# Optimization experiments

Measured on AMD Instinct MI355X. Metric: run time of the kernel, lower is better.

The kernel has to match this reference:

```python
import jax, jax.numpy as jnp
import numpy as np

D_MODEL = 1024
N_HEADS = 16
D_H = D_MODEL // N_HEADS
B, T = 4, 2048
NEG_INF = jnp.finfo(jnp.float32).min


def setup_inputs() -> dict:
    key = jax.random.key(0)
    ks = jax.random.split(key, 9)
    s = 1.0 / np.sqrt(D_MODEL)
    inp = {
        "x": jax.random.normal(ks[0], (B, T, D_MODEL), dtype=jnp.float32),
        "pad_mask": jnp.zeros((B, T), dtype=bool),
        "Wq": jax.random.uniform(ks[1], (D_MODEL, D_MODEL), jnp.float32, -s, s),
        "bq": jax.random.uniform(ks[2], (D_MODEL,), jnp.float32, -s, s),
        "Wk": jax.random.uniform(ks[3], (D_MODEL, D_MODEL), jnp.float32, -s, s),
        "bk": jax.random.uniform(ks[4], (D_MODEL,), jnp.float32, -s, s),
        "Wv": jax.random.uniform(ks[5], (D_MODEL, D_MODEL), jnp.float32, -s, s),
        "bv": jax.random.uniform(ks[6], (D_MODEL,), jnp.float32, -s, s),
        "Wo": jax.random.uniform(ks[7], (D_MODEL, D_MODEL), jnp.float32, -s, s),
        "bo": jax.random.uniform(ks[8], (D_MODEL,), jnp.float32, -s, s),
    }
    return inp


def reference(x, pad_mask, Wq, bq, Wk, bk, Wv, bv, Wo, bo):
    b, t, _ = x.shape
    # torch Linear: y = x @ W.T + b
    def proj(W, bias):
        y = jnp.einsum("btd,ed->bte", x, W) + bias
        return y.reshape(b, t, N_HEADS, D_H).transpose(0, 2, 1, 3)  # (B,H,T,d_h)

    Q, K, V = proj(Wq, bq), proj(Wk, bk), proj(Wv, bv)
    S = jnp.einsum("bhqd,bhkd->bhqk", Q, K) / jnp.sqrt(jnp.float32(D_H))
    causal = jnp.triu(jnp.ones((t, t), dtype=bool), k=1)[None, None]
    S = jnp.where(causal, NEG_INF, S)
    S = jnp.where(pad_mask[:, None, None, :], NEG_INF, S)
    A = jax.nn.softmax(S, axis=-1)
    Y = jnp.einsum("bhqk,bhkd->bhqd", A, V)
    Y = Y.transpose(0, 2, 1, 3).reshape(b, t, D_MODEL)
    O = jnp.einsum("btd,ed->bte", Y, Wo) + bo
    return O
```

## Files before the change

kernel.cpp:

```cpp
#include <hip/hip_runtime.h>
#include <stdint.h>
#include <stddef.h>

#define Tq 2048
#define DM 1024

typedef unsigned short u16;
typedef __bf16 bf16x8 __attribute__((ext_vector_type(8)));
typedef float f32x4 __attribute__((ext_vector_type(4)));
typedef unsigned short u16x8 __attribute__((ext_vector_type(8)));
typedef unsigned short u16x4 __attribute__((ext_vector_type(4)));

__device__ __forceinline__ float bf2f(u16 h) {
    union { unsigned int u; float f; } c; c.u = ((unsigned int)h) << 16; return c.f;
}
__device__ __forceinline__ u16 f2bf(float f) {
    union { float f; unsigned int u; } c; c.f = f;
    unsigned int u = c.u;
    return (u16)((u + 0x7fffu + ((u >> 16) & 1u)) >> 16);
}

#define GLD(gp, lp) __builtin_amdgcn_global_load_lds(                                  \
        (const __attribute__((address_space(1))) void*)(gp),                           \
        (__attribute__((address_space(3))) void*)(lp), 16, 0, 0)

__device__ __forceinline__ int sniff_fp32(const u16* xs) {
    const int lane = threadIdx.x & 63;
    const u16 u = xs[lane];
    const int e = (u >> 7) & 0xFF;
    unsigned long long m = __ballot(e >= 160);
    return __popcll(m) >= 4;
}

__device__ __forceinline__ void cvt_body(const void* src, u16* dst, int i0, int fmt) {
    if (fmt) {
        const float* s = (const float*)src;
        float4 a = *(const float4*)(s + i0);
        float4 b = *(const float4*)(s + i0 + 4);
        u16x8 o;
        o[0] = f2bf(a.x); o[1] = f2bf(a.y); o[2] = f2bf(a.z); o[3] = f2bf(a.w);
        o[4] = f2bf(b.x); o[5] = f2bf(b.y); o[6] = f2bf(b.z); o[7] = f2bf(b.w);
        *(u16x8*)(dst + i0) = o;
    } else {
        *(u16x8*)(dst + i0) = *(const u16x8*)((const u16*)src + i0);
    }
}

__global__ void cvt_all(const void* __restrict__ x,
                        const void* s0, const void* s1, const void* s2, const void* s3,
                        const void* t0, const void* t1, const void* t2, const void* t3,
                        u16* __restrict__ xc, u16* __restrict__ dstW, float* __restrict__ dstB,
                        const u16* __restrict__ xs, int* flag) {
    const int fmt = sniff_fp32(xs);
    int bx = blockIdx.x;
    if (bx < 4096) {
        if (bx == 0 && threadIdx.x == 0) *flag = fmt;
        const int i0 = (bx * 256 + threadIdx.x) * 8;
        cvt_body(x, xc, i0, fmt);
    } else {
        bx -= 4096;
        const int wsel = bx >> 9;
        const int bi   = bx & 511;
        const void* s = (wsel == 0) ? s0 : (wsel == 1) ? s1 : (wsel == 2) ? s2 : s3;
        u16* d = dstW + (size_t)wsel * (DM * DM);
        const int i0 = (bi * 256 + threadIdx.x) * 8;
        cvt_body(s, d, i0, fmt);
        if (bi == 0) {
            const void* bs = (wsel == 0) ? t0 : (wsel == 1) ? t1 : (wsel == 2) ? t2 : t3;
            float* db = dstB + (size_t)wsel * DM;
            const int j0 = threadIdx.x * 4;
            if (fmt) {
                *(float4*)(db + j0) = *(const float4*)((const float*)bs + j0);
            } else {
                const u16* ss = (const u16*)bs;
                db[j0+0] = bf2f(ss[j0+0]); db[j0+1] = bf2f(ss[j0+1]);
                db[j0+2] = bf2f(ss[j0+2]); db[j0+3] = bf2f(ss[j0+3]);
            }
        }
    }
}

__global__ __launch_bounds__(256, 2) void gemm_bt(
    const u16* __restrict__ A,
    const u16* __restrict__ W0, const u16* __restrict__ W1, const u16* __restrict__ W2,
    const float* __restrict__ b0, const float* __restrict__ b1, const float* __restrict__ b2,
    u16* o0, u16* o1, u16* o2,
    const int* __restrict__ flag, int mode)
{
    __shared__ u16 Alds[128 * 64];
    __shared__ u16 Blds[128 * 64];

    const int K = DM;
    const int i = blockIdx.x;
    const int j = blockIdx.y;
    const int which = (mode == 0) ? (j >> 3) : 0;
    const u16* W      = (which == 0) ? W0 : (which == 1) ? W1 : W2;
    const float* bias = (which == 0) ? b0 : (which == 1) ? b1 : b2;
    u16* out          = (which == 0) ? o0 : (which == 1) ? o1 : o2;
    const int jn = (mode == 0) ? (j & 7) : j;
    const int m0 = i * 128, n0 = jn * 128;
    const int ofmt = (mode == 1) ? *flag : 0;

    const int tid = threadIdx.x;
    const int w = tid >> 6, lane = tid & 63;
    const int l4 = lane & 15, quad = lane >> 4;
    const int wrow = w >> 1, wcol = w & 1;

    f32x4 acc[4][4] = {};

    for (int k0 = 0; k0 < K; k0 += 64) {
        __syncthreads();
#pragma unroll
        for (int c = 0; c < 4; ++c) {
            const int u   = w * 1024 + c * 4096;
            const int off = u + lane * 16;
            const int row = off >> 7;
            const int col = (off & 127) >> 1;
            GLD(A + (size_t)(m0 + row) * K + k0 + col, (char*)Alds + u);
            GLD(W + (size_t)(n0 + row) * K + k0 + col, (char*)Blds + u);
        }
        __syncthreads();
#pragma unroll
        for (int c = 0; c < 2; ++c) {
            bf16x8 af[4], bfr[4];
#pragma unroll
            for (int r = 0; r < 4; ++r)
                af[r] = *(const bf16x8*)&Alds[(wrow*64 + r*16 + l4) * 64 + c*32 + quad*8];
#pragma unroll
            for (int n = 0; n < 4; ++n)
                bfr[n] = *(const bf16x8*)&Blds[(wcol*64 + n*16 + l4) * 64 + c*32 + quad*8];
#pragma unroll
            for (int r = 0; r < 4; ++r)
#pragma unroll
                for (int n = 0; n < 4; ++n)
                    acc[r][n] = __builtin_amdgcn_mfma_f32_16x16x32_bf16(af[r], bfr[n], acc[r][n], 0, 0, 0);
        }
    }

#pragma unroll
    for (int n = 0; n < 4; ++n) {
        const int col = n0 + wcol*64 + n*16 + l4;
        const float bv = bias[col];
#pragma unroll
        for (int r = 0; r < 4; ++r) {
            const int mb = m0 + wrow*64 + r*16 + quad*4;
            if (mode == 0 && which == 2) {
                const int b = mb >> 11, t0 = mb & 2047;
                const int h = col >> 6, d = col & 63;
                u16x4 pk;
#pragma unroll
                for (int reg = 0; reg < 4; ++reg) pk[reg] = f2bf(acc[r][n][reg] + bv);
                *(u16x4*)&out[((size_t)(b*16 + h) * 64 + d) * 2048 + t0] = pk;
            } else {
#pragma unroll
                for (int reg = 0; reg < 4; ++reg) {
                    const int m = mb + reg;
                    const float val = acc[r][n][reg] + bv;
                    if (mode == 0) {
                        const int b = m >> 11, t = m & 2047;
                        const int h = col >> 6, d = col & 63;
                        out[(size_t)((b*16 + h) * 2048 + t) * 64 + d] = f2bf(val);
                    } else if (ofmt) {
                        ((float*)out)[(size_t)m * DM + col] = val;
                    } else {
                        out[(size_t)m * DM + col] = f2bf(val);
                    }
                }
            }
        }
    }
}

#define LSTR 72

__global__ __launch_bounds__(256, 2) void attn4(
    const u16* __restrict__ Qb, const u16* __restrict__ Kb, const u16* __restrict__ VT,
    const unsigned char* __restrict__ pad,
    u16* __restrict__ Y)
{
    __shared__ u16 Klds[2][64 * LSTR];
    __shared__ u16 Vtl [2][64 * LSTR];
    __shared__ u16 Pl  [4][64 * LSTR];
    __shared__ unsigned char padl[2][64];

    const int nb = blockIdx.y;
    const int bh = blockIdx.x;
    const int b = bh >> 4, h = bh & 15;
    const u16* Qp  = Qb + (size_t)bh * (Tq * 64);
    const u16* Kp  = Kb + (size_t)bh * (Tq * 64);
    const u16* VTp = VT + (size_t)bh * (64 * Tq);

    const int tid = threadIdx.x;
    const int w = tid >> 6, lane = tid & 63;
    const int l4 = lane & 15, quad = lane >> 4;

    const int qt[4] = { nb, nb + 8, 23 - nb, 31 - nb };

    bf16x8 qf[4][2];
#pragma unroll
    for (int g = 0; g < 4; ++g) {
        const u16* r = Qp + (size_t)(qt[g] * 64 + w * 16 + l4) * 64 + quad * 8;
        qf[g][0] = *(const bf16x8*)r;
        qf[g][1] = *(const bf16x8*)(r + 32);
    }

    f32x4 o[4][4] = {};
    float l[4][4] = {};

    const int srow = tid >> 2;
    const int sc   = (tid & 3) * 16;

    u16x8 kr0, kr1, vr0, vr1; unsigned char pr = 0;
    {
        const u16* kg = Kp + (size_t)srow * 64 + sc;
        kr0 = *(const u16x8*)kg; kr1 = *(const u16x8*)(kg + 8);
        const u16* vg = VTp + (size_t)srow * Tq + sc;
        vr0 = *(const u16x8*)vg; vr1 = *(const u16x8*)(vg + 8);
        if (tid < 64) pr = pad[(size_t)b * Tq + tid];
    }
    *(u16x8*)&Klds[0][srow * LSTR + sc]     = kr0;
    *(u16x8*)&Klds[0][srow * LSTR + sc + 8] = kr1;
    *(u16x8*)&Vtl [0][srow * LSTR + sc]     = vr0;
    *(u16x8*)&Vtl [0][srow * LSTR + sc + 8] = vr1;
    if (tid < 64) padl[0][tid] = pr;

    const float SC = 0.18033688011112042f;
    const int ktmax = qt[3];

    for (int kt = 0; kt <= ktmax; ++kt) {
        const int cur = kt & 1;
        const int k0 = kt * 64;
        __syncthreads();
        if (kt < ktmax) {
            const u16* kg = Kp + (size_t)(k0 + 64 + srow) * 64 + sc;
            kr0 = *(const u16x8*)kg; kr1 = *(const u16x8*)(kg + 8);
            const u16* vg = VTp + (size_t)srow * Tq + k0 + 64 + sc;
            vr0 = *(const u16x8*)vg; vr1 = *(const u16x8*)(vg + 8);
            if (tid < 64) pr = pad[(size_t)b * Tq + k0 + 64 + tid];
        }

        const bool anypad = __any((int)(padl[cur][lane] != 0));

        bf16x8 kf[2][4];
#pragma unroll
        for (int c = 0; c < 2; ++c)
#pragma unroll
            for (int n = 0; n < 4; ++n)
                kf[c][n] = *(const bf16x8*)&Klds[cur][(n * 16 + l4) * LSTR + c * 32 + quad * 8];

#pragma unroll
        for (int g = 0; g < 4; ++g) {
            if (kt > qt[g]) continue;
            f32x4 sacc[4] = {};
            __builtin_amdgcn_s_setprio(1);
#pragma unroll
            for (int c = 0; c < 2; ++c)
#pragma unroll
                for (int n = 0; n < 4; ++n)
                    sacc[n] = __builtin_amdgcn_mfma_f32_16x16x32_bf16(qf[g][c], kf[c][n], sacc[n], 0, 0, 0);
            __builtin_amdgcn_s_setprio(0);
            u16* Pg = &Pl[g][0];
            if (kt == qt[g] || anypad) {
                bool pm[4];
#pragma unroll
                for (int n = 0; n < 4; ++n) pm[n] = (padl[cur][n * 16 + l4] != 0);
                const int qr = qt[g] * 64 + w * 16 + quad * 4;
#pragma unroll
                for (int r = 0; r < 4; ++r) {
                    float rs = 0.f;
#pragma unroll
                    for (int n = 0; n < 4; ++n) {
                        const int kgi = k0 + n * 16 + l4;
                        const bool msk = (kgi > qr + r) || pm[n];
                        const float p = msk ? 0.0f : exp2f(sacc[n][r] * SC);
                        rs += p;
                        *(__bf16*)&Pg[(w * 16 + quad * 4 + r) * LSTR + n * 16 + l4] = (__bf16)p;
                    }
                    l[g][r] += rs;
                }
            } else {
#pragma unroll
                for (int r = 0; r < 4; ++r) {
                    float rs = 0.f;
#pragma unroll
                    for (int n = 0; n < 4; ++n) {
                        const float p = exp2f(sacc[n][r] * SC);
                        rs += p;
                        *(__bf16*)&Pg[(w * 16 + quad * 4 + r) * LSTR + n * 16 + l4] = (__bf16)p;
                    }
                    l[g][r] += rs;
                }
            }
        }

        bf16x8 vf[2][4];
#pragma unroll
        for (int c = 0; c < 2; ++c)
#pragma unroll
            for (int t = 0; t < 4; ++t)
                vf[c][t] = *(const bf16x8*)&Vtl[cur][(t * 16 + l4) * LSTR + c * 32 + quad * 8];

#pragma unroll
        for (int g = 0; g < 4; ++g) {
            if (kt > qt[g]) continue;
            __builtin_amdgcn_s_setprio(1);
#pragma unroll
            for (int c = 0; c < 2; ++c) {
                bf16x8 pf = *(const bf16x8*)&Pl[g][(w * 16 + l4) * LSTR + c * 32 + quad * 8];
#pragma unroll
                for (int t = 0; t < 4; ++t)
                    o[g][t] = __builtin_amdgcn_mfma_f32_16x16x32_bf16(pf, vf[c][t], o[g][t], 0, 0, 0);
            }
            __builtin_amdgcn_s_setprio(0);
        }

        if (kt < ktmax) {
            *(u16x8*)&Klds[cur ^ 1][srow * LSTR + sc]     = kr0;
            *(u16x8*)&Klds[cur ^ 1][srow * LSTR + sc + 8] = kr1;
            *(u16x8*)&Vtl [cur ^ 1][srow * LSTR + sc]     = vr0;
            *(u16x8*)&Vtl [cur ^ 1][srow * LSTR + sc + 8] = vr1;
            if (tid < 64) padl[cur ^ 1][tid] = pr;
        }
    }

#pragma unroll
    for (int g = 0; g < 4; ++g)
#pragma unroll
        for (int r = 0; r < 4; ++r)
#pragma unroll
            for (int s = 1; s < 16; s <<= 1)
                l[g][r] += __shfl_xor(l[g][r], s);

#pragma unroll
    for (int g = 0; g < 4; ++g)
#pragma unroll
        for (int r = 0; r < 4; ++r) {
            const float inv = 1.0f / l[g][r];
            u16* y = Y + (size_t)(b * Tq + (qt[g] * 64 + w * 16 + quad * 4 + r)) * DM + h * 64;
#pragma unroll
            for (int t = 0; t < 4; ++t)
                *(__bf16*)&y[t * 16 + l4] = (__bf16)(o[g][t][r] * inv);
        }
}

extern "C" void kernel_launch(void* const* d_in, const int* in_sizes, int n_in,
                              void* d_out, int out_size, void* d_ws, size_t ws_size,
                              hipStream_t stream) {
    const void* x  = d_in[0];
    const unsigned char* pad = (const unsigned char*)d_in[1];
    const void* Wq = d_in[2];
    const void* bq = d_in[3];
    const void* Wk = d_in[4];
    const void* bk = d_in[5];
    const void* Wv = d_in[6];
    const void* bv = d_in[7];
    const void* Wo = d_in[8];
    const void* bo = d_in[9];
    const u16* xs = (const u16*)x;

    const size_t NEL = (size_t)8192 * 1024;
    const size_t WEL = (size_t)1024 * 1024;

    int* flag   = (int*)d_ws;
    u16* base16 = (u16*)((char*)d_ws + 256);
    u16* xc     = base16;
    u16* Wc     = base16 + NEL;
    float* bf_  = (float*)(base16 + NEL + 4*WEL);
    u16* Qb     = (u16*)(bf_ + 4096);
    u16* Kb     = Qb + NEL;
    u16* VT     = Kb + NEL;
    u16* Yb     = xc;

    cvt_all<<<dim3(6144), 256, 0, stream>>>(x, Wq, Wk, Wv, Wo, bq, bk, bv, bo,
                                            xc, Wc, bf_, xs, flag);

    gemm_bt<<<dim3(64, 24), 256, 0, stream>>>(xc, Wc, Wc + WEL, Wc + 2*WEL,
                                              bf_, bf_ + 1024, bf_ + 2048,
                                              Qb, Kb, VT, flag, 0);
    attn4<<<dim3(64, 8), 256, 0, stream>>>(Qb, Kb, VT, pad, Yb);
    gemm_bt<<<dim3(64, 8), 256, 0, stream>>>(Yb, Wc + 3*WEL, Wc + 3*WEL, Wc + 3*WEL,
                                             bf_ + 3072, bf_ + 3072, bf_ + 3072,
                                             (u16*)d_out, nullptr, nullptr, flag, 1);
}
```

Baseline: 278.1 us.

## Rewrite projection GEMM with 128x256 tiles, double-buffered LDS, swizzle, and folded Q scale

Replaces the 128x128 single-buffered GEMM with a 512-thread 128x256-tile kernel. It prefetches the next K-tiles into a second LDS buffer via global_load_lds with explicit vmcnt waits, and XOR-swizzles LDS columns to cut bank conflicts. The softmax scale is folded into the Q projection epilogue, which removes a multiply per score in the attention kernel. The larger tile gives more reuse per block but needs 96KB of LDS, which may limit occupancy and leaves fewer blocks for the output projection.

```diff
diff --git a/kernel.cpp b/kernel.cpp
--- a/kernel.cpp
+++ b/kernel.cpp
@@ -80,92 +80,128 @@
     }
 }
 
-__global__ __launch_bounds__(256, 2) void gemm_bt(
+#define NT 16
+
+__global__ __launch_bounds__(512, 2) void gemm256(
     const u16* __restrict__ A,
     const u16* __restrict__ W0, const u16* __restrict__ W1, const u16* __restrict__ W2,
     const float* __restrict__ b0, const float* __restrict__ b1, const float* __restrict__ b2,
     u16* o0, u16* o1, u16* o2,
     const int* __restrict__ flag, int mode)
 {
-    __shared__ u16 Alds[128 * 64];
-    __shared__ u16 Blds[128 * 64];
+    __shared__ u16 LB[2][24576];
 
     const int K = DM;
-    const int i = blockIdx.x;
     const int j = blockIdx.y;
-    const int which = (mode == 0) ? (j >> 3) : 0;
-    const u16* W      = (which == 0) ? W0 : (which == 1) ? W1 : W2;
+    const int which = (mode == 0) ? (j >> 2) : 0;
+    const u16* Wp     = (which == 0) ? W0 : (which == 1) ? W1 : W2;
     const float* bias = (which == 0) ? b0 : (which == 1) ? b1 : b2;
     u16* out          = (which == 0) ? o0 : (which == 1) ? o1 : o2;
-    const int jn = (mode == 0) ? (j & 7) : j;
-    const int m0 = i * 128, n0 = jn * 128;
+    const int jn = (mode == 0) ? (j & 3) : j;
+    const int m0 = blockIdx.x * 128, n0 = jn * 256;
+
+    const int tid  = threadIdx.x;
+    const int w    = tid >> 6, lane = tid & 63;
+    const int wm   = w >> 2, wn = w & 3;
+    const int l4   = lane & 15, quad = lane >> 4;
+    const int rsub = lane >> 3;
+    const int colE = ((lane & 7) ^ rsub) << 3;
+
+#define STAGE(kt, bf) do {                                                              \
+        const int k0s = (kt) * 64;                                                      \
+        _Pragma("unroll")                                                               \
+        for (int c = 0; c < 2; ++c) {                                                   \
+            const int row = c * 64 + w * 8 + rsub;                                      \
+            GLD(A + (size_t)(m0 + row) * K + k0s + colE,                                \
+                (char*)&LB[bf][0] + c * 8192 + w * 1024);                               \
+        }                                                                               \
+        _Pragma("unroll")                                                               \
+        for (int c = 0; c < 4; ++c) {                                                   \
+            const int row = c * 64 + w * 8 + rsub;                                      \
+            GLD(Wp + (size_t)(n0 + row) * K + k0s + colE,                               \
+                (char*)&LB[bf][0] + 16384 + c * 8192 + w * 1024);                       \
+        }                                                                               \
+    } while (0)
+
+    f32x4 acc[4][4] = {};
+
+    STAGE(0, 0);
+    STAGE(1, 1);
+    asm volatile("s_waitcnt vmcnt(6)" ::: "memory");
+    __syncthreads();
+
+    for (int t = 0; t < NT; ++t) {
+        const int cur = t & 1;
+        const u16* Ab = &LB[cur][0];
+        const u16* Bb = &LB[cur][8192];
+        const int swz = (l4 & 7) << 3;
+
+        bf16x8 af[2][4], bf[2][4];
+#pragma unroll
+        for (int kc = 0; kc < 2; ++kc) {
+            const int kq = (kc * 32 + quad * 8);
+#pragma unroll
+            for (int m = 0; m < 4; ++m)
+                af[kc][m] = *(const bf16x8*)&Ab[(wm * 64 + m * 16 + l4) * 64 + (kq ^ swz)];
+#pragma unroll
+            for (int n = 0; n < 4; ++n)
+                bf[kc][n] = *(const bf16x8*)&Bb[(wn * 64 + n * 16 + l4) * 64 + (kq ^ swz)];
+        }
+        __builtin_amdgcn_s_setprio(1);
+#pragma unroll
+        for (int kc = 0; kc < 2; ++kc)
+#pragma unroll
+            for (int m = 0; m < 4; ++m)
+#pragma unroll
+                for (int n = 0; n < 4; ++n)
+                    acc[m][n] = __builtin_amdgcn_mfma_f32_16x16x32_bf16(af[kc][m], bf[kc][n], acc[m][n], 0, 0, 0);
+        __builtin_amdgcn_s_setprio(0);
+
+        __syncthreads();
+        if (t + 2 < NT) {
+            STAGE(t + 2, cur);
+        }
+        if (t + 1 < NT) {
+            if (t + 2 < NT) asm volatile("s_waitcnt vmcnt(6)" ::: "memory");
+            else            asm volatile("s_waitcnt vmcnt(0)" ::: "memory");
+            __syncthreads();
+        }
+    }
+#undef STAGE
+
     const int ofmt = (mode == 1) ? *flag : 0;
-
-    const int tid = threadIdx.x;
-    const int w = tid >> 6, lane = tid & 63;
-    const int l4 = lane & 15, quad = lane >> 4;
-    const int wrow = w >> 1, wcol = w & 1;
-
-    f32x4 acc[4][4] = {};
-
-    for (int k0 = 0; k0 < K; k0 += 64) {
-        __syncthreads();
-#pragma unroll
-        for (int c = 0; c < 4; ++c) {
-            const int u   = w * 1024 + c * 4096;
-            const int off = u + lane * 16;
-            const int row = off >> 7;
-            const int col = (off & 127) >> 1;
-            GLD(A + (size_t)(m0 + row) * K + k0 + col, (char*)Alds + u);
-            GLD(W + (size_t)(n0 + row) * K + k0 + col, (char*)Blds + u);
-        }
-        __syncthreads();
-#pragma unroll
-        for (int c = 0; c < 2; ++c) {
-            bf16x8 af[4], bfr[4];
-#pragma unroll
-            for (int r = 0; r < 4; ++r)
-                af[r] = *(const bf16x8*)&Alds[(wrow*64 + r*16 + l4) * 64 + c*32 + quad*8];
-#pragma unroll
-            for (int n = 0; n < 4; ++n)
-                bfr[n] = *(const bf16x8*)&Blds[(wcol*64 + n*16 + l4) * 64 + c*32 + quad*8];
-#pragma unroll
-            for (int r = 0; r < 4; ++r)
-#pragma unroll
-                for (int n = 0; n < 4; ++n)
-                    acc[r][n] = __builtin_amdgcn_mfma_f32_16x16x32_bf16(af[r], bfr[n], acc[r][n], 0, 0, 0);
-        }
-    }
+    const float SCQ = 0.18033688011112042f;
 
 #pragma unroll
     for (int n = 0; n < 4; ++n) {
-        const int col = n0 + wcol*64 + n*16 + l4;
-        const float bv = bias[col];
-#pragma unroll
-        for (int r = 0; r < 4; ++r) {
-            const int mb = m0 + wrow*64 + r*16 + quad*4;
-            if (mode == 0 && which == 2) {
-                const int b = mb >> 11, t0 = mb & 2047;
-                const int h = col >> 6, d = col & 63;
-                u16x4 pk;
-#pragma unroll
-                for (int reg = 0; reg < 4; ++reg) pk[reg] = f2bf(acc[r][n][reg] + bv);
-                *(u16x4*)&out[((size_t)(b*16 + h) * 64 + d) * 2048 + t0] = pk;
+        const int colw = n0 + wn * 64 + n * 16 + l4;
+        const float bv = bias[colw];
+#pragma unroll
+        for (int m = 0; m < 4; ++m) {
+            const int mb = m0 + wm * 64 + m * 16 + quad * 4;
+            if (mode == 0) {
+                const int bb = mb >> 11, t0 = mb & 2047;
+                const int h = colw >> 6, d = colw & 63;
+                if (which == 2) {
+                    u16x4 pk;
+#pragma unroll
+                    for (int reg = 0; reg < 4; ++reg) pk[reg] = f2bf(acc[m][n][reg] + bv);
+                    *(u16x4*)&out[((size_t)(bb * 16 + h) * 64 + d) * 2048 + t0] = pk;
+                } else {
+                    const float s = (which == 0) ? SCQ : 1.0f;
+#pragma unroll
+                    for (int reg = 0; reg < 4; ++reg)
+                        out[(size_t)((bb * 16 + h) * 2048 + (t0 + reg)) * 64 + d] =
+                            f2bf((acc[m][n][reg] + bv) * s);
+                }
+            } else if (ofmt) {
+#pragma unroll
+                for (int reg = 0; reg < 4; ++reg)
+                    ((float*)out)[(size_t)(mb + reg) * DM + colw] = acc[m][n][reg] + bv;
             } else {
 #pragma unroll
-                for (int reg = 0; reg < 4; ++reg) {
-                    const int m = mb + reg;
-                    const float val = acc[r][n][reg] + bv;
-                    if (mode == 0) {
-                        const int b = m >> 11, t = m & 2047;
-                        const int h = col >> 6, d = col & 63;
-                        out[(size_t)((b*16 + h) * 2048 + t) * 64 + d] = f2bf(val);
-                    } else if (ofmt) {
-                        ((float*)out)[(size_t)m * DM + col] = val;
-                    } else {
-                        out[(size_t)m * DM + col] = f2bf(val);
-                    }
-                }
+                for (int reg = 0; reg < 4; ++reg)
+                    out[(size_t)(mb + reg) * DM + colw] = f2bf(acc[m][n][reg] + bv);
             }
         }
     }
@@ -224,7 +260,6 @@
     *(u16x8*)&Vtl [0][srow * LSTR + sc + 8] = vr1;
     if (tid < 64) padl[0][tid] = pr;
 
-    const float SC = 0.18033688011112042f;
     const int ktmax = qt[3];
 
     for (int kt = 0; kt <= ktmax; ++kt) {
@@ -272,7 +307,7 @@
                     for (int n = 0; n < 4; ++n) {
                         const int kgi = k0 + n * 16 + l4;
                         const bool msk = (kgi > qr + r) || pm[n];
-                        const float p = msk ? 0.0f : exp2f(sacc[n][r] * SC);
+                        const float p = msk ? 0.0f : exp2f(sacc[n][r]);
                         rs += p;
                         *(__bf16*)&Pg[(w * 16 + quad * 4 + r) * LSTR + n * 16 + l4] = (__bf16)p;
                     }
@@ -284,7 +319,7 @@
                     float rs = 0.f;
 #pragma unroll
                     for (int n = 0; n < 4; ++n) {
-                        const float p = exp2f(sacc[n][r] * SC);
+                        const float p = exp2f(sacc[n][r]);
                         rs += p;
                         *(__bf16*)&Pg[(w * 16 + quad * 4 + r) * LSTR + n * 16 + l4] = (__bf16)p;
                     }
@@ -374,11 +409,11 @@
     cvt_all<<<dim3(6144), 256, 0, stream>>>(x, Wq, Wk, Wv, Wo, bq, bk, bv, bo,
                                             xc, Wc, bf_, xs, flag);
 
-    gemm_bt<<<dim3(64, 24), 256, 0, stream>>>(xc, Wc, Wc + WEL, Wc + 2*WEL,
+    gemm256<<<dim3(64, 12), 512, 0, stream>>>(xc, Wc, Wc + WEL, Wc + 2*WEL,
                                               bf_, bf_ + 1024, bf_ + 2048,
                                               Qb, Kb, VT, flag, 0);
     attn4<<<dim3(64, 8), 256, 0, stream>>>(Qb, Kb, VT, pad, Yb);
-    gemm_bt<<<dim3(64, 8), 256, 0, stream>>>(Yb, Wc + 3*WEL, Wc + 3*WEL, Wc + 3*WEL,
+    gemm256<<<dim3(64, 4), 512, 0, stream>>>(Yb, Wc + 3*WEL, Wc + 3*WEL, Wc + 3*WEL,
                                              bf_ + 3072, bf_ + 3072, bf_ + 3072,
                                              (u16*)d_out, nullptr, nullptr, flag, 1);
 }
```

After: 285.0 us. 2.5% more time.
